# Kernel optimization log

Measured on AMD Instinct MI355X. Metric: run time of the kernel, lower is better.

## Reference

```python
import jax, jax.numpy as jnp
import numpy as np

# Body-part joint index groups, in the exact concat order of the torch forward:
# p1 torso, p1 left_hand, p1 left_leg, p1 right_hand, p1 right_leg, then same +25 for person 2.
_P1 = [
    [0, 1, 2, 3, 20],
    [8, 9, 10, 11, 23, 24],
    [16, 17, 18, 19],
    [4, 5, 6, 7, 21, 22],
    [12, 13, 14, 15],
]
PARTS = [np.array(g) for g in _P1] + [np.array(g) + 25 for g in _P1]


def setup_inputs() -> dict:
    key = jax.random.key(0)
    k_x, k_w1, k_w2 = jax.random.split(key, 3)
    N, C, T, V = 64, 256, 64, 50
    H = C // 16  # hidden width of the squeeze-excite MLP
    x = jax.random.normal(k_x, (N, C, T, V), dtype=jnp.float32)
    W1 = jax.random.normal(k_w1, (10, H, C), dtype=jnp.float32) * (2.0 / C) ** 0.5
    b1 = jnp.zeros((10, H), dtype=jnp.float32)
    W2 = jax.random.normal(k_w2, (10, C, H), dtype=jnp.float32) * (2.0 / H) ** 0.5
    b2 = jnp.zeros((10, C), dtype=jnp.float32)
    return {"x": x, "W1": W1, "b1": b1, "W2": W2, "b2": b2}


def reference(x, W1, b1, W2, b2):
    # x: [N, C, T, V=50]. For each of 10 fixed body parts: gather joints,
    # global avg & max pool over (T, joints), tiny 2-layer MLP on each pooled
    # vector, sigmoid(avg_path + max_path) channel gate, re-weight the slice.
    outs = []
    for p, idx in enumerate(PARTS):
        xs = x[:, :, :, idx]                       # [N, C, T, k]
        avg = jnp.mean(xs, axis=(2, 3))            # [N, C]
        mx = jnp.max(xs, axis=(2, 3))              # [N, C]

        def mlp(v):
            h = jax.nn.relu(v @ W1[p].T + b1[p])   # [N, H]
            return h @ W2[p].T + b2[p]             # [N, C]

        gate = jax.nn.sigmoid(mlp(avg) + mlp(mx))  # [N, C]
        outs.append(xs * gate[:, :, None, None])
    # Concatenate along the joint dim in part order (reorders joints, as in torch).
    return jnp.concatenate(outs, axis=3)           # [N, C, T, 50]
```

## Files before the change

### kernel.cpp

```cpp
#include <hip/hip_runtime.h>

#define N_  64
#define C_  256
#define T_  64
#define V_  50
#define H_  16
#define NP_ 10
#define ROW_ (T_ * V_)
#define NC_  (N_ * C_)
#define NPC_ (N_ * NP_ * C_)

typedef float f32x4 __attribute__((ext_vector_type(4)));

constexpr int PART_OF_V[V_] = {
    0,0,0,0, 3,3,3,3, 1,1,1,1, 4,4,4,4, 2,2,2,2, 0, 3,3, 1,1,
    5,5,5,5, 8,8,8,8, 6,6,6,6, 9,9,9,9, 7,7,7,7, 5, 8,8, 6,6};

constexpr float INV_CNT[NP_] = {
    1.f/320, 1.f/384, 1.f/256, 1.f/384, 1.f/256,
    1.f/320, 1.f/384, 1.f/256, 1.f/384, 1.f/256};

__device__ const int SRC_V[V_] = {
    0,1,2,3,20,  8,9,10,11,23,24,  16,17,18,19,  4,5,6,7,21,22,  12,13,14,15,
    25,26,27,28,45,  33,34,35,36,48,49,  41,42,43,44,  29,30,31,32,46,47,  37,38,39,40};
__device__ const int PART_W[V_] = {
    0,0,0,0,0, 1,1,1,1,1,1, 2,2,2,2, 3,3,3,3,3,3, 4,4,4,4,
    5,5,5,5,5, 6,6,6,6,6,6, 7,7,7,7, 8,8,8,8,8,8, 9,9,9,9};

__global__ __launch_bounds__(256) void reduce_kernel(
    const float* __restrict__ x,
    float* __restrict__ avg_out,
    float* __restrict__ max_out) {
    __shared__ float lds[4][ROW_];
    const int wave = threadIdx.x >> 6;
    const int lane = threadIdx.x & 63;
    const int row  = blockIdx.x * 4 + wave;

    const float4* xr4 = (const float4*)(x + (size_t)row * ROW_);
    float4* l4 = (float4*)lds[wave];
    #pragma unroll
    for (int j = 0; j < 12; ++j) l4[lane + 64 * j] = xr4[lane + 64 * j];
    if (lane < 32) l4[lane + 768] = xr4[lane + 768];
    __syncthreads();

    const float* l = lds[wave] + lane * V_;
    float s[NP_], m[NP_];
    #pragma unroll
    for (int p = 0; p < NP_; ++p) { s[p] = 0.f; m[p] = -__builtin_huge_valf(); }
    #pragma unroll
    for (int v = 0; v < V_; ++v) {
        float val = l[v];
        s[PART_OF_V[v]] += val;
        m[PART_OF_V[v]] = fmaxf(m[PART_OF_V[v]], val);
    }

    #pragma unroll
    for (int p = 0; p < NP_; ++p) {
        #pragma unroll
        for (int off = 32; off > 0; off >>= 1) {
            s[p] += __shfl_xor(s[p], off);
            m[p] = fmaxf(m[p], __shfl_xor(m[p], off));
        }
    }

    if (lane == 0) {
        const int n = row >> 8, c = row & 255;
        #pragma unroll
        for (int p = 0; p < NP_; ++p) {
            avg_out[(n * NP_ + p) * C_ + c] = s[p] * INV_CNT[p];
            max_out[(n * NP_ + p) * C_ + c] = m[p];
        }
    }
}

__global__ __launch_bounds__(256) void mlp_kernel(
    const float* __restrict__ avg, const float* __restrict__ mx,
    const float* __restrict__ W1, const float* __restrict__ b1,
    const float* __restrict__ W2, const float* __restrict__ b2,
    float* __restrict__ gate) {
    const int np = blockIdx.x;
    const int p  = np % NP_;
    __shared__ float vec[2][C_];
    __shared__ float partial[256];
    __shared__ float hsum[H_];

    const int t = threadIdx.x;
    vec[0][t] = avg[np * C_ + t];
    vec[1][t] = mx[np * C_ + t];
    __syncthreads();

    const int which = t & 1, h = (t >> 1) & 15, chunk = t >> 5;
    const float* w1row = W1 + (p * H_ + h) * C_ + chunk * 32;
    const float* vv = vec[which] + chunk * 32;
    float acc = 0.f;
    #pragma unroll
    for (int k = 0; k < 32; ++k) acc += w1row[k] * vv[k];
    partial[t] = acc;
    __syncthreads();

    if (t < 32) {
        float a = b1[p * H_ + h];
        #pragma unroll
        for (int j = 0; j < 8; ++j) a += partial[t + 32 * j];
        a = fmaxf(a, 0.f);
        if (which == 0) hsum[h] = a;
    }
    __syncthreads();
    if (t < 32 && (t & 1) == 1) {
        float a = b1[p * H_ + h];
        #pragma unroll
        for (int j = 0; j < 8; ++j) a += partial[t + 32 * j];
        hsum[h] += fmaxf(a, 0.f);
    }
    __syncthreads();

    const float4* w2row = (const float4*)(W2 + (p * C_ + t) * H_);
    float z = 2.f * b2[p * C_ + t];
    #pragma unroll
    for (int q = 0; q < 4; ++q) {
        float4 w = w2row[q];
        z += w.x * hsum[4*q] + w.y * hsum[4*q+1] + w.z * hsum[4*q+2] + w.w * hsum[4*q+3];
    }
    gate[np * C_ + t] = 1.f / (1.f + __expf(-z));
}

__device__ __forceinline__ void scatter4(float* __restrict__ ly,
                                         const float2* __restrict__ tab,
                                         int u, float4 d) {
    const int base = u * 4;
    int t = base / V_;
    int v = base - t * V_;
    float vals[4] = {d.x, d.y, d.z, d.w};
    #pragma unroll
    for (int k = 0; k < 4; ++k) {
        float2 tv = tab[v];
        ly[t * V_ + __float_as_int(tv.x)] = vals[k] * tv.y;
        if (++v == V_) { v = 0; ++t; }
    }
}

__global__ __launch_bounds__(256) void scale_kernel(
    const float* __restrict__ x, const float* __restrict__ gate,
    float* __restrict__ out) {
    __shared__ float  ly[ROW_];
    __shared__ float2 tab[V_];

    const int row = blockIdx.x;
    const int n = row >> 8, c = row & 255;
    const int tid = threadIdx.x;

    if (tid < V_) {
        const int w = tid;
        const int v = SRC_V[w];
        const float g = gate[(n * NP_ + PART_W[w]) * C_ + c];
        tab[v] = make_float2(__int_as_float(w), g);
    }

    const float4* src = (const float4*)(x + (size_t)row * ROW_);
    float4 d0 = src[tid];
    float4 d1 = src[tid + 256];
    float4 d2 = src[tid + 512];
    float4 d3;
    if (tid < 32) d3 = src[tid + 768];
    __syncthreads();

    scatter4(ly, tab, tid,       d0);
    scatter4(ly, tab, tid + 256, d1);
    scatter4(ly, tab, tid + 512, d2);
    if (tid < 32) scatter4(ly, tab, tid + 768, d3);
    __syncthreads();

    const f32x4* ly4 = (const f32x4*)ly;
    f32x4* dst = (f32x4*)(out + (size_t)row * ROW_);
    __builtin_nontemporal_store(ly4[tid],       &dst[tid]);
    __builtin_nontemporal_store(ly4[tid + 256], &dst[tid + 256]);
    __builtin_nontemporal_store(ly4[tid + 512], &dst[tid + 512]);
    if (tid < 32)
        __builtin_nontemporal_store(ly4[tid + 768], &dst[tid + 768]);
}

extern "C" void kernel_launch(void* const* d_in, const int* in_sizes, int n_in,
                              void* d_out, int out_size, void* d_ws, size_t ws_size,
                              hipStream_t stream) {
    const float* x  = (const float*)d_in[0];
    const float* W1 = (const float*)d_in[1];
    const float* b1 = (const float*)d_in[2];
    const float* W2 = (const float*)d_in[3];
    const float* b2 = (const float*)d_in[4];
    float* out = (float*)d_out;

    float* avg  = (float*)d_ws;
    float* mx   = avg + NPC_;
    float* gate = mx + NPC_;

    reduce_kernel<<<NC_ / 4, 256, 0, stream>>>(x, avg, mx);
    mlp_kernel<<<N_ * NP_, 256, 0, stream>>>(avg, mx, W1, b1, W2, b2, gate);
    scale_kernel<<<NC_, 256, 0, stream>>>(x, gate, out);
}
```

Before: 386.8 us.

## Swizzle LDS gather in scale kernel and use LDS cross-lane reduction

The scale kernel now writes input rows linearly into LDS with an XOR swizzle and has each thread gather its output elements through a per-joint offset/gate table. This replaces the scattered LDS writes that needed per-element index division and caused bank conflicts. The reduce kernel reads LDS as float2 and replaces the 10×2 shuffle butterfly reductions with a transpose through LDS, where 20 lanes each reduce one part. The LDS reduction adds a barrier and serial 32-step loops on a few lanes, which trades shuffle instructions for lower lane utilisation.

```diff
diff --git a/kernel.cpp b/kernel.cpp
--- a/kernel.cpp
+++ b/kernel.cpp
@@ -16,7 +16,7 @@
     0,0,0,0, 3,3,3,3, 1,1,1,1, 4,4,4,4, 2,2,2,2, 0, 3,3, 1,1,
     5,5,5,5, 8,8,8,8, 6,6,6,6, 9,9,9,9, 7,7,7,7, 5, 8,8, 6,6};
 
-constexpr float INV_CNT[NP_] = {
+__device__ const float INV_CNT_D[NP_] = {
     1.f/320, 1.f/384, 1.f/256, 1.f/384, 1.f/256,
     1.f/320, 1.f/384, 1.f/256, 1.f/384, 1.f/256};
 
@@ -43,32 +43,43 @@
     if (lane < 32) l4[lane + 768] = xr4[lane + 768];
     __syncthreads();
 
-    const float* l = lds[wave] + lane * V_;
+    const float2* l2 = (const float2*)(lds[wave] + lane * V_);
     float s[NP_], m[NP_];
     #pragma unroll
     for (int p = 0; p < NP_; ++p) { s[p] = 0.f; m[p] = -__builtin_huge_valf(); }
     #pragma unroll
-    for (int v = 0; v < V_; ++v) {
-        float val = l[v];
-        s[PART_OF_V[v]] += val;
-        m[PART_OF_V[v]] = fmaxf(m[PART_OF_V[v]], val);
-    }
-
+    for (int j = 0; j < 25; ++j) {
+        float2 q = l2[j];
+        s[PART_OF_V[2*j]]   += q.x;
+        m[PART_OF_V[2*j]]    = fmaxf(m[PART_OF_V[2*j]], q.x);
+        s[PART_OF_V[2*j+1]] += q.y;
+        m[PART_OF_V[2*j+1]]  = fmaxf(m[PART_OF_V[2*j+1]], q.y);
+    }
+
+    float* buf = lds[wave];
     #pragma unroll
     for (int p = 0; p < NP_; ++p) {
-        #pragma unroll
-        for (int off = 32; off > 0; off >>= 1) {
-            s[p] += __shfl_xor(s[p], off);
-            m[p] = fmaxf(m[p], __shfl_xor(m[p], off));
-        }
-    }
-
-    if (lane == 0) {
+        buf[p * 66 + lane]          = s[p];
+        buf[(p + 10) * 66 + lane]   = m[p];
+    }
+    __syncthreads();
+
+    if (lane < 20) {
         const int n = row >> 8, c = row & 255;
-        #pragma unroll
-        for (int p = 0; p < NP_; ++p) {
-            avg_out[(n * NP_ + p) * C_ + c] = s[p] * INV_CNT[p];
-            max_out[(n * NP_ + p) * C_ + c] = m[p];
+        const float2* b2 = (const float2*)(lds[wave] + lane * 66);
+        if (lane < 10) {
+            float2 a = b2[0];
+            float acc = a.x + a.y;
+            #pragma unroll
+            for (int j = 1; j < 32; ++j) { float2 q = b2[j]; acc += q.x + q.y; }
+            avg_out[(n * NP_ + lane) * C_ + c] = acc * INV_CNT_D[lane];
+        } else {
+            const int p = lane - 10;
+            float2 a = b2[0];
+            float acc = fmaxf(a.x, a.y);
+            #pragma unroll
+            for (int j = 1; j < 32; ++j) { float2 q = b2[j]; acc = fmaxf(acc, fmaxf(q.x, q.y)); }
+            max_out[(n * NP_ + p) * C_ + c] = acc;
         }
     }
 }
@@ -124,26 +135,11 @@
     gate[np * C_ + t] = 1.f / (1.f + __expf(-z));
 }
 
-__device__ __forceinline__ void scatter4(float* __restrict__ ly,
-                                         const float2* __restrict__ tab,
-                                         int u, float4 d) {
-    const int base = u * 4;
-    int t = base / V_;
-    int v = base - t * V_;
-    float vals[4] = {d.x, d.y, d.z, d.w};
-    #pragma unroll
-    for (int k = 0; k < 4; ++k) {
-        float2 tv = tab[v];
-        ly[t * V_ + __float_as_int(tv.x)] = vals[k] * tv.y;
-        if (++v == V_) { v = 0; ++t; }
-    }
-}
-
 __global__ __launch_bounds__(256) void scale_kernel(
     const float* __restrict__ x, const float* __restrict__ gate,
     float* __restrict__ out) {
-    __shared__ float  ly[ROW_];
-    __shared__ float2 tab[V_];
+    __shared__ float  lx[ROW_];
+    __shared__ float4 tq[25];
 
     const int row = blockIdx.x;
     const int n = row >> 8, c = row & 255;
@@ -151,32 +147,58 @@
 
     if (tid < V_) {
         const int w = tid;
-        const int v = SRC_V[w];
         const float g = gate[(n * NP_ + PART_W[w]) * C_ + c];
-        tab[v] = make_float2(__int_as_float(w), g);
+        const int dsv = SRC_V[w] - w;
+        float* t4 = (float*)&tq[w >> 1];
+        t4[(w & 1) * 2 + 0] = __int_as_float(dsv);
+        t4[(w & 1) * 2 + 1] = g;
     }
 
     const float4* src = (const float4*)(x + (size_t)row * ROW_);
     float4 d0 = src[tid];
     float4 d1 = src[tid + 256];
     float4 d2 = src[tid + 512];
-    float4 d3;
+    float4 d3 = {};
     if (tid < 32) d3 = src[tid + 768];
-    __syncthreads();
-
-    scatter4(ly, tab, tid,       d0);
-    scatter4(ly, tab, tid + 256, d1);
-    scatter4(ly, tab, tid + 512, d2);
-    if (tid < 32) scatter4(ly, tab, tid + 768, d3);
-    __syncthreads();
-
-    const f32x4* ly4 = (const f32x4*)ly;
+
+    {
+        float vals[16] = {d0.x,d0.y,d0.z,d0.w, d1.x,d1.y,d1.z,d1.w,
+                          d2.x,d2.y,d2.z,d2.w, d3.x,d3.y,d3.z,d3.w};
+        #pragma unroll
+        for (int r = 0; r < 4; ++r) {
+            if (r == 3 && tid >= 32) break;
+            const int f0 = (tid + 256 * r) * 4;
+            #pragma unroll
+            for (int k = 0; k < 4; ++k) {
+                const int f = f0 + k;
+                lx[f ^ ((f >> 5) & 3)] = vals[r * 4 + k];
+            }
+        }
+    }
+    __syncthreads();
+
     f32x4* dst = (f32x4*)(out + (size_t)row * ROW_);
-    __builtin_nontemporal_store(ly4[tid],       &dst[tid]);
-    __builtin_nontemporal_store(ly4[tid + 256], &dst[tid + 256]);
-    __builtin_nontemporal_store(ly4[tid + 512], &dst[tid + 512]);
-    if (tid < 32)
-        __builtin_nontemporal_store(ly4[tid + 768], &dst[tid + 768]);
+    int w0 = (tid << 2) % 50u;
+    #pragma unroll
+    for (int rep = 0; rep < 4; ++rep) {
+        if (rep == 3 && tid >= 32) break;
+        const int u  = tid + 256 * rep;
+        const int e0 = u * 4;
+        int wB = w0 + 2; if (wB >= V_) wB -= V_;
+        const float4 tA = tq[w0 >> 1];
+        const float4 tB = tq[wB >> 1];
+        const int f0 = e0 + 0 + __float_as_int(tA.x);
+        const int f1 = e0 + 1 + __float_as_int(tA.z);
+        const int f2 = e0 + 2 + __float_as_int(tB.x);
+        const int f3 = e0 + 3 + __float_as_int(tB.z);
+        f32x4 o;
+        o.x = lx[f0 ^ ((f0 >> 5) & 3)] * tA.y;
+        o.y = lx[f1 ^ ((f1 >> 5) & 3)] * tA.w;
+        o.z = lx[f2 ^ ((f2 >> 5) & 3)] * tB.y;
+        o.w = lx[f3 ^ ((f3 >> 5) & 3)] * tB.w;
+        __builtin_nontemporal_store(o, &dst[u]);
+        w0 += 24; if (w0 >= V_) w0 -= V_;
+    }
 }
 
 extern "C" void kernel_launch(void* const* d_in, const int* in_sizes, int n_in,
```

Measured after the change: 386.8 us. No clear change (-0.0%).
